# Optimization experiments

Measured on AMD Instinct MI355X. Metric: run time of the kernel, lower is better.

The kernel has to match this reference:

```python
import jax, jax.numpy as jnp
import numpy as np

NUM_LAYER = 5
EMB = 300
N_NODES = 100000
N_EDGES = 250000
BN_EPS = 1e-5


def setup_inputs() -> dict:
    key = jax.random.key(0)
    ks = jax.random.split(key, 12)
    s = 0.05
    inp = {
        "x": jax.random.randint(ks[0], (N_NODES, 2), 0, 3),
        "edge_index": jax.random.randint(ks[1], (2, N_EDGES), 0, N_NODES),
        "edge_attr": jax.random.randint(ks[2], (N_EDGES, 2), 0, 3),
        # node-feature embedding tables
        "x_emb1": jax.random.normal(ks[3], (120, EMB), jnp.float32) * s,
        "x_emb2": jax.random.normal(ks[4], (3, EMB), jnp.float32) * s,
        # per-layer edge embedding tables (bond type=6, bond direction=3)
        "e_emb1": jax.random.normal(ks[5], (NUM_LAYER, 6, EMB), jnp.float32) * s,
        "e_emb2": jax.random.normal(ks[6], (NUM_LAYER, 3, EMB), jnp.float32) * s,
        # per-layer GIN MLP: Linear(D,2D) -> ReLU -> Linear(2D,D); weights stored (out,in)
        "w1": jax.random.normal(ks[7], (NUM_LAYER, 2 * EMB, EMB), jnp.float32) * s,
        "b1": jnp.zeros((NUM_LAYER, 2 * EMB), jnp.float32),
        "w2": jax.random.normal(ks[8], (NUM_LAYER, EMB, 2 * EMB), jnp.float32) * s,
        "b2": jnp.zeros((NUM_LAYER, EMB), jnp.float32),
        # per-layer BatchNorm1d affine params (training-mode batch stats)
        "gamma": jnp.ones((NUM_LAYER, EMB), jnp.float32),
        "beta": jnp.zeros((NUM_LAYER, EMB), jnp.float32),
    }
    return inp


def reference(x, edge_index, edge_attr, x_emb1, x_emb2, e_emb1, e_emb2, w1, b1, w2, b2, gamma, beta):
    n = x.shape[0]
    # input node embedding: atom type + chirality tag
    h = x_emb1[x[:, 0]] + x_emb2[x[:, 1]]  # [N, D]

    # add self loops (self-loop edge_attr = [4, 0])
    loop = jnp.arange(n, dtype=edge_index.dtype)
    src = jnp.concatenate([edge_index[0], loop])  # [E+N]
    dst = jnp.concatenate([edge_index[1], loop])
    ea0 = jnp.concatenate([edge_attr[:, 0], jnp.full((n,), 4, edge_attr.dtype)])
    ea1 = jnp.concatenate([edge_attr[:, 1], jnp.zeros((n,), edge_attr.dtype)])

    for l in range(NUM_LAYER):
        e = e_emb1[l][ea0] + e_emb2[l][ea1]           # [E+N, D] edge embeddings
        msg = h[src] + e                               # gather + message
        agg = jax.ops.segment_sum(msg, dst, num_segments=n)  # scatter-add aggregate
        hid = jnp.maximum(agg @ w1[l].T + b1[l], 0.0)  # GIN MLP
        h2 = hid @ w2[l].T + b2[l]
        # BatchNorm1d (training-mode batch statistics, biased variance)
        mu = h2.mean(axis=0)
        var = jnp.mean((h2 - mu) ** 2, axis=0)
        h2 = (h2 - mu) * jax.lax.rsqrt(var + BN_EPS) * gamma[l] + beta[l]
        if l < NUM_LAYER - 1:
            h2 = jnp.maximum(h2, 0.0)  # ReLU (dropout ratio = 0)
        h = h2

    # JK == 'last'
    return h
```

## Files before the change

### kernel.cpp

```cpp
#include <hip/hip_runtime.h>
#include <hip/hip_bf16.h>

#define DD 300
#define C4 75
#define AGS 320
#define BN_EPS 1e-5f

typedef _Float16 f16x8 __attribute__((ext_vector_type(8)));
typedef float f32x4 __attribute__((ext_vector_type(4)));

union PackH4 { _Float16 h[4]; uint2 u; };

__device__ __forceinline__ void gld_lds16(const void* g, void* lds) {
    __builtin_amdgcn_global_load_lds(
        (const __attribute__((address_space(1))) void*)g,
        (__attribute__((address_space(3))) void*)lds, 16, 0, 0);
}

__global__ __launch_bounds__(256) void embed_kernel(
    const int* __restrict__ x, const float* __restrict__ emb1,
    const float* __restrict__ emb2, float* __restrict__ h, int hs, int total4)
{
    int i = blockIdx.x * 256 + threadIdx.x;
    if (i >= total4) return;
    int node = i / C4, chunk = i - node * C4;
    int a = x[2 * node], b = x[2 * node + 1];
    int c = chunk << 2;
    float4 v1 = *(const float4*)(emb1 + (size_t)a * DD + c);
    float4 v2 = *(const float4*)(emb2 + (size_t)b * DD + c);
    float4 r;
    r.x = v1.x + v2.x; r.y = v1.y + v2.y; r.z = v1.z + v2.z; r.w = v1.w + v2.w;
    *(float4*)(h + (size_t)node * hs + c) = r;
}

__global__ __launch_bounds__(256) void build_ec_kernel(
    const float* __restrict__ e1, const float* __restrict__ e2, float* __restrict__ ec)
{
    int gid = blockIdx.x * 256 + threadIdx.x;
    if (gid >= 5 * 18 * DD) return;
    int l = gid / (18 * DD);
    int rem = gid - l * 18 * DD;
    int combo = rem / DD;
    int c = rem - combo * DD;
    int a0 = combo / 3, a1 = combo - a0 * 3;
    ec[gid] = e1[(size_t)l * 6 * DD + a0 * DD + c] + e2[(size_t)l * 3 * DD + a1 * DD + c];
}

__global__ __launch_bounds__(256) void deg_kernel(
    const int* __restrict__ ei, int* __restrict__ deg, int E)
{
    int e = blockIdx.x * 256 + threadIdx.x;
    if (e >= E) return;
    atomicAdd(&deg[ei[E + e]], 1);
}

__global__ __launch_bounds__(256) void scan1_kernel(
    const int* __restrict__ deg, int* __restrict__ pre, int* __restrict__ blockSum, int n)
{
    __shared__ int sa[256], sb[256];
    int t = threadIdx.x;
    int base = blockIdx.x * 1024 + t * 4;
    int v0 = (base + 0 < n) ? deg[base + 0] : 0;
    int v1 = (base + 1 < n) ? deg[base + 1] : 0;
    int v2 = (base + 2 < n) ? deg[base + 2] : 0;
    int v3 = (base + 3 < n) ? deg[base + 3] : 0;
    int tot = v0 + v1 + v2 + v3;
    sa[t] = tot;
    __syncthreads();
    int* src = sa; int* dst = sb;
    for (int off = 1; off < 256; off <<= 1) {
        int v = src[t];
        if (t >= off) v += src[t - off];
        dst[t] = v;
        __syncthreads();
        int* tmp = src; src = dst; dst = tmp;
    }
    int incl = src[t];
    int excl = incl - tot;
    if (base + 0 < n) pre[base + 0] = excl;
    if (base + 1 < n) pre[base + 1] = excl + v0;
    if (base + 2 < n) pre[base + 2] = excl + v0 + v1;
    if (base + 3 < n) pre[base + 3] = excl + v0 + v1 + v2;
    if (t == 255) blockSum[blockIdx.x] = incl;
}

__global__ __launch_bounds__(256) void scan2_kernel(int* __restrict__ blockSum, int nb)
{
    __shared__ int sa[256], sb[256];
    int t = threadIdx.x;
    int v = (t < nb) ? blockSum[t] : 0;
    sa[t] = v;
    __syncthreads();
    int* src = sa; int* dst = sb;
    for (int off = 1; off < 256; off <<= 1) {
        int x = src[t];
        if (t >= off) x += src[t - off];
        dst[t] = x;
        __syncthreads();
        int* tmp = src; src = dst; dst = tmp;
    }
    if (t < nb) blockSum[t] = src[t] - v;
}

__global__ __launch_bounds__(256) void scan3_kernel(
    const int* __restrict__ pre, const int* __restrict__ blockSum,
    int* __restrict__ rowPtr, int* __restrict__ cursor, int n, int E)
{
    int idx = blockIdx.x * 256 + threadIdx.x;
    if (idx > n) return;
    int v = (idx < n) ? pre[idx] + blockSum[idx >> 10] : E;
    rowPtr[idx] = v;
    if (idx < n) cursor[idx] = v;
}

__global__ __launch_bounds__(256) void fill_kernel(
    const int* __restrict__ ei, const int* __restrict__ ea,
    int* __restrict__ cursor, int* __restrict__ edges, int E)
{
    int e = blockIdx.x * 256 + threadIdx.x;
    if (e >= E) return;
    int src = ei[e];
    int dst = ei[E + e];
    int combo = ea[2 * e] * 3 + ea[2 * e + 1];
    int slot = atomicAdd(&cursor[dst], 1);
    edges[slot] = src | (combo << 18);
}

__global__ __launch_bounds__(256) void gather_kernel(
    const float* __restrict__ h, int hs, const int* __restrict__ rowPtr,
    const int* __restrict__ edges, const float* __restrict__ ec,
    const float* __restrict__ scale, const float* __restrict__ shift, int use_affine,
    _Float16* __restrict__ agg, int n)
{
    int gid = blockIdx.x * 256 + threadIdx.x;
    int node = gid / C4, ch = gid - node * C4;
    if (node >= n) return;
    int c = ch << 2;
    float4 sc, sh;
    if (use_affine) {
        sc = *(const float4*)(scale + c);
        sh = *(const float4*)(shift + c);
    }
    float4 acc = *(const float4*)(h + (size_t)node * hs + c);
    if (use_affine) {
        acc.x = fmaxf(fmaf(sc.x, acc.x, sh.x), 0.f);
        acc.y = fmaxf(fmaf(sc.y, acc.y, sh.y), 0.f);
        acc.z = fmaxf(fmaf(sc.z, acc.z, sh.z), 0.f);
        acc.w = fmaxf(fmaf(sc.w, acc.w, sh.w), 0.f);
    }
    float4 es = *(const float4*)(ec + 12 * DD + c);
    acc.x += es.x; acc.y += es.y; acc.z += es.z; acc.w += es.w;

    int start = rowPtr[node], end = rowPtr[node + 1];
    for (int e = start; e < end; ++e) {
        int pk = edges[e];
        int src = pk & 0x3FFFF;
        int combo = pk >> 18;
        float4 hv = *(const float4*)(h + (size_t)src * hs + c);
        if (use_affine) {
            hv.x = fmaxf(fmaf(sc.x, hv.x, sh.x), 0.f);
            hv.y = fmaxf(fmaf(sc.y, hv.y, sh.y), 0.f);
            hv.z = fmaxf(fmaf(sc.z, hv.z, sh.z), 0.f);
            hv.w = fmaxf(fmaf(sc.w, hv.w, sh.w), 0.f);
        }
        float4 ev = *(const float4*)(ec + combo * DD + c);
        acc.x += hv.x + ev.x;
        acc.y += hv.y + ev.y;
        acc.z += hv.z + ev.z;
        acc.w += hv.w + ev.w;
    }
    PackH4 p;
    p.h[0] = (_Float16)acc.x;
    p.h[1] = (_Float16)acc.y;
    p.h[2] = (_Float16)acc.z;
    p.h[3] = (_Float16)acc.w;
    *(uint2*)(agg + (size_t)node * AGS + c) = p.u;
}

__global__ __launch_bounds__(256) void convert_w_kernel(
    const float* __restrict__ w, _Float16* __restrict__ wf,
    int rows, int cols, int rowsP, int colsP)
{
    int gid = blockIdx.x * 256 + threadIdx.x;
    int total = 5 * rowsP * colsP;
    if (gid >= total) return;
    int l = gid / (rowsP * colsP);
    int rem = gid - l * (rowsP * colsP);
    int r = rem / colsP;
    int k = rem - r * colsP;
    float v = (r < rows && k < cols) ? w[((size_t)l * rows + r) * cols + k] : 0.f;
    wf[gid] = (_Float16)v;
}

template <bool OUT_F16, bool DO_STATS>
__global__ __launch_bounds__(512, 4) void mfma_gemm_lds(
    const _Float16* __restrict__ A, const _Float16* __restrict__ W,
    const float* __restrict__ bias,
    _Float16* __restrict__ outH, float* __restrict__ outF,
    float* __restrict__ sum, float* __restrict__ sumsq,
    int M, int Kp, int outStride, int outN, int nCol)
{
    __shared__ __attribute__((aligned(16))) unsigned short sA[128 * 64];
    __shared__ __attribute__((aligned(16))) unsigned short sB[128 * 64];

    const int bid = blockIdx.x;
    const int group = bid / (8 * nCol);
    const int within = bid - group * 8 * nCol;
    const int rowT = group * 8 + (within & 7);
    const int colT = within >> 3;
    const int bm = rowT << 7;
    const int bn = colT << 7;

    const int tid = threadIdx.x;
    const int lane = tid & 63, wv = tid >> 6;
    const int wy = wv & 3, wx = wv >> 2;
    const int quad = lane >> 4, l16 = lane & 15;

    const int r8 = lane >> 3;
    const int chv = (lane & 7) ^ r8;

    f32x4 acc[2][4] = {};

    for (int k0 = 0; k0 < Kp; k0 += 64) {
        __syncthreads();
#pragma unroll
        for (int j = 0; j < 2; ++j) {
            int rloc = wv * 16 + j * 8 + r8;
            gld_lds16(A + (size_t)(bm + rloc) * Kp + k0 + chv * 8,
                      &sA[(wv * 16 + j * 8) * 64]);
        }
#pragma unroll
        for (int j = 0; j < 2; ++j) {
            int rloc = wv * 16 + j * 8 + r8;
            gld_lds16(W + (size_t)(bn + rloc) * Kp + k0 + chv * 8,
                      &sB[(wv * 16 + j * 8) * 64]);
        }
        __syncthreads();
#pragma unroll
        for (int kk = 0; kk < 2; ++kk) {
            f16x8 a[2], b[4];
#pragma unroll
            for (int i = 0; i < 2; ++i) {
                int rA = wy * 32 + i * 16 + l16;
                int slotA = (kk * 4 + quad) ^ (rA & 7);
                a[i] = *(const f16x8*)&sA[rA * 64 + slotA * 8];
            }
#pragma unroll
            for (int j = 0; j < 4; ++j) {
                int rB = wx * 64 + j * 16 + l16;
                int slotB = (kk * 4 + quad) ^ (rB & 7);
                b[j] = *(const f16x8*)&sB[rB * 64 + slotB * 8];
            }
#pragma unroll
            for (int i = 0; i < 2; ++i)
#pragma unroll
                for (int j = 0; j < 4; ++j)
                    acc[i][j] = __builtin_amdgcn_mfma_f32_16x16x32_f16(
                        a[i], b[j], acc[i][j], 0, 0, 0);
        }
    }

#pragma unroll
    for (int j = 0; j < 4; ++j) {
        int col = bn + wx * 64 + j * 16 + l16;
        float bv = (col < outN) ? bias[col] : 0.f;
        float cs = 0.f, cq = 0.f;
#pragma unroll
        for (int i = 0; i < 2; ++i) {
            int rowBase = bm + wy * 32 + i * 16 + (quad << 2);
#pragma unroll
            for (int r = 0; r < 4; ++r) {
                int row = rowBase + r;
                if (row >= M) continue;
                float v = acc[i][j][r] + bv;
                if constexpr (DO_STATS) { if (col < outN) { cs += v; cq += v * v; } }
                if constexpr (OUT_F16) {
                    float o = (col < outN) ? fmaxf(v, 0.f) : 0.f;
                    outH[(size_t)row * outStride + col] = (_Float16)o;
                } else {
                    if (col < outStride) outF[(size_t)row * outStride + col] = v;
                }
            }
        }
        if constexpr (DO_STATS) {
            cs += __shfl_down(cs, 32); cq += __shfl_down(cq, 32);
            cs += __shfl_down(cs, 16); cq += __shfl_down(cq, 16);
            if (quad == 0 && col < outN) {
                atomicAdd(&sum[col], cs);
                atomicAdd(&sumsq[col], cq);
            }
        }
    }
}

__global__ void finalize_kernel(
    const float* __restrict__ sum, const float* __restrict__ sumsq,
    const float* __restrict__ gamma, const float* __restrict__ beta,
    float* __restrict__ scale, float* __restrict__ shift, float inv_n)
{
    int c = threadIdx.x;
    if (c < DD) {
        float mu = sum[c] * inv_n;
        float var = sumsq[c] * inv_n - mu * mu;
        float inv = rsqrtf(var + BN_EPS);
        float sc = gamma[c] * inv;
        scale[c] = sc;
        shift[c] = fmaf(-mu, sc, beta[c]);
    }
}

__global__ __launch_bounds__(256) void apply_kernel(
    const float* __restrict__ h, int hs, const float* __restrict__ scale,
    const float* __restrict__ shift, float* __restrict__ out, int total4)
{
    int i = blockIdx.x * 256 + threadIdx.x;
    if (i >= total4) return;
    int node = i / C4;
    int c = (i - node * C4) << 2;
    float4 v = *(const float4*)(h + (size_t)node * hs + c);
    float4 r;
    r.x = fmaf(scale[c + 0], v.x, shift[c + 0]);
    r.y = fmaf(scale[c + 1], v.y, shift[c + 1]);
    r.z = fmaf(scale[c + 2], v.z, shift[c + 2]);
    r.w = fmaf(scale[c + 3], v.w, shift[c + 3]);
    ((float4*)out)[i] = r;
}

extern "C" void kernel_launch(void* const* d_in, const int* in_sizes, int n_in,
                              void* d_out, int out_size, void* d_ws, size_t ws_size,
                              hipStream_t stream)
{
    const int*   x      = (const int*)d_in[0];
    const int*   ei     = (const int*)d_in[1];
    const int*   ea     = (const int*)d_in[2];
    const float* x_emb1 = (const float*)d_in[3];
    const float* x_emb2 = (const float*)d_in[4];
    const float* e_emb1 = (const float*)d_in[5];
    const float* e_emb2 = (const float*)d_in[6];
    const float* w1     = (const float*)d_in[7];
    const float* b1     = (const float*)d_in[8];
    const float* w2     = (const float*)d_in[9];
    const float* b2     = (const float*)d_in[10];
    const float* gamma  = (const float*)d_in[11];
    const float* beta   = (const float*)d_in[12];

    const int n = in_sizes[0] / 2;
    const int E = in_sizes[1] / 2;
    const int nRowT = (n + 127) / 128;
    const int nRowTP = ((nRowT + 7) / 8) * 8;
    const int MpA = nRowTP * 128;
    const int Kp1 = AGS, Kp2 = 640;
    const int NP1 = 640, NP2 = 384;

    char* p = (char*)d_ws;
    auto alloc = [&](size_t bytes) -> void* {
        void* r = (void*)p;
        p += (bytes + 255) & ~(size_t)255;
        return r;
    };
    _Float16* agg  = (_Float16*)alloc((size_t)MpA * Kp1 * 2);
    _Float16* hid  = (_Float16*)alloc((size_t)MpA * Kp2 * 2);
    _Float16* w1f  = (_Float16*)alloc((size_t)5 * NP1 * Kp1 * 2);
    _Float16* w2f  = (_Float16*)alloc((size_t)5 * NP2 * Kp2 * 2);
    float* ec     = (float*)alloc((size_t)5 * 18 * DD * 4);
    int*   deg    = (int*)alloc((size_t)n * 4);
    int*   rowPtr = (int*)alloc((size_t)(n + 1) * 4);
    int*   cursor = (int*)alloc((size_t)n * 4);
    int*   blockSum = (int*)alloc(256 * 4);
    int*   edges  = (int*)alloc((size_t)E * 4);
    float* sum   = (float*)alloc(320 * 4);
    float* sumsq = (float*)alloc(320 * 4);
    float* scale = (float*)alloc(320 * 4);
    float* shift = (float*)alloc(320 * 4);

    const size_t used = (size_t)(p - (char*)d_ws);
    const size_t hBytes = (size_t)n * 320 * 4;
    float* h;
    int HS;
    if (ws_size >= used + hBytes) {
        h = (float*)alloc(hBytes);
        HS = 320;
    } else {
        h = (float*)d_out;
        HS = DD;
    }

    const int total4 = n * C4;
    const int nb = (n + 1023) / 1024;

    {
        convert_w_kernel<<<(5 * NP1 * Kp1 + 255) / 256, 256, 0, stream>>>(w1, w1f, 600, 300, NP1, Kp1);
        convert_w_kernel<<<(5 * NP2 * Kp2 + 255) / 256, 256, 0, stream>>>(w2, w2f, 300, 600, NP2, Kp2);
        build_ec_kernel<<<(5 * 18 * DD + 255) / 256, 256, 0, stream>>>(e_emb1, e_emb2, ec);
        hipMemsetAsync(deg, 0, (size_t)n * 4, stream);
        deg_kernel<<<(E + 255) / 256, 256, 0, stream>>>(ei, deg, E);
        scan1_kernel<<<nb, 256, 0, stream>>>(deg, cursor , blockSum, n);
        scan2_kernel<<<1, 256, 0, stream>>>(blockSum, nb);
        scan3_kernel<<<(n + 256) / 256, 256, 0, stream>>>(cursor, blockSum, rowPtr, deg , n, E);
        fill_kernel<<<(E + 255) / 256, 256, 0, stream>>>(ei, ea, deg, edges, E);
        hipMemsetAsync(agg, 0, (size_t)MpA * Kp1 * 2, stream);
        embed_kernel<<<(total4 + 255) / 256, 256, 0, stream>>>(x, x_emb1, x_emb2, h, HS, total4);
    }

    const int gatherTotal = n * C4;
    const int nCol1 = NP1 / 128;
    const int nCol2 = NP2 / 128;
    const int g1 = nRowTP * nCol1;
    const int g2 = nRowTP * nCol2;

    for (int l = 0; l < 5; l++) {
        hipMemsetAsync(sum, 0, 2 * 320 * sizeof(float), stream);
        gather_kernel<<<(gatherTotal + 255) / 256, 256, 0, stream>>>(
            h, HS, rowPtr, edges, ec + (size_t)l * 18 * DD, scale, shift, l > 0 ? 1 : 0,
            agg, n);
        mfma_gemm_lds<true, false><<<g1, 512, 0, stream>>>(
            agg, w1f + (size_t)l * NP1 * Kp1,
            b1 + (size_t)l * 600, hid, nullptr, nullptr, nullptr,
            n, Kp1, Kp2, 600, nCol1);
        mfma_gemm_lds<false, true><<<g2, 512, 0, stream>>>(
            hid, w2f + (size_t)l * NP2 * Kp2,
            b2 + (size_t)l * 300, nullptr, h, sum, sumsq,
            n, Kp2, HS, 300, nCol2);
        finalize_kernel<<<1, 320, 0, stream>>>(sum, sumsq, gamma + (size_t)l * DD,
                                               beta + (size_t)l * DD, scale, shift,
                                               1.0f / (float)n);
    }
    apply_kernel<<<(total4 + 255) / 256, 256, 0, stream>>>(h, HS, scale, shift,
                                                           (float*)d_out, total4);
}
```

Measured before the change: 1.875 ms.

## Double-buffer LDS tiles in MFMA GEMM to overlap global loads with compute

Splits the GEMM K-loop into stage and compute steps over two LDS buffers, so the next K tile is prefetched with direct global-to-LDS loads while the current tile feeds the MFMAs. Explicit vmcnt waits and raw barriers replace the two __syncthreads per iteration. LDS use per block doubles to 64KB and the occupancy hint drops from 4 to 2 blocks per CU, which may reduce latency hiding across blocks.

```diff
diff --git a/kernel.cpp b/kernel.cpp
--- a/kernel.cpp
+++ b/kernel.cpp
@@ -193,15 +193,15 @@
 }
 
 template <bool OUT_F16, bool DO_STATS>
-__global__ __launch_bounds__(512, 4) void mfma_gemm_lds(
+__global__ __launch_bounds__(512, 2) void mfma_gemm_lds(
     const _Float16* __restrict__ A, const _Float16* __restrict__ W,
     const float* __restrict__ bias,
     _Float16* __restrict__ outH, float* __restrict__ outF,
     float* __restrict__ sum, float* __restrict__ sumsq,
     int M, int Kp, int outStride, int outN, int nCol)
 {
-    __shared__ __attribute__((aligned(16))) unsigned short sA[128 * 64];
-    __shared__ __attribute__((aligned(16))) unsigned short sB[128 * 64];
+    __shared__ __attribute__((aligned(16))) unsigned short sA[2][128 * 64];
+    __shared__ __attribute__((aligned(16))) unsigned short sB[2][128 * 64];
 
     const int bid = blockIdx.x;
     const int group = bid / (8 * nCol);
@@ -221,21 +221,22 @@
 
     f32x4 acc[2][4] = {};
 
-    for (int k0 = 0; k0 < Kp; k0 += 64) {
-        __syncthreads();
+    auto STAGE = [&](int buf, int k0) {
 #pragma unroll
         for (int j = 0; j < 2; ++j) {
             int rloc = wv * 16 + j * 8 + r8;
             gld_lds16(A + (size_t)(bm + rloc) * Kp + k0 + chv * 8,
-                      &sA[(wv * 16 + j * 8) * 64]);
+                      &sA[buf][(wv * 16 + j * 8) * 64]);
         }
 #pragma unroll
         for (int j = 0; j < 2; ++j) {
             int rloc = wv * 16 + j * 8 + r8;
             gld_lds16(W + (size_t)(bn + rloc) * Kp + k0 + chv * 8,
-                      &sB[(wv * 16 + j * 8) * 64]);
-        }
-        __syncthreads();
+                      &sB[buf][(wv * 16 + j * 8) * 64]);
+        }
+    };
+
+    auto COMPUTE = [&](int buf) {
 #pragma unroll
         for (int kk = 0; kk < 2; ++kk) {
             f16x8 a[2], b[4];
@@ -243,13 +244,13 @@
             for (int i = 0; i < 2; ++i) {
                 int rA = wy * 32 + i * 16 + l16;
                 int slotA = (kk * 4 + quad) ^ (rA & 7);
-                a[i] = *(const f16x8*)&sA[rA * 64 + slotA * 8];
+                a[i] = *(const f16x8*)&sA[buf][rA * 64 + slotA * 8];
             }
 #pragma unroll
             for (int j = 0; j < 4; ++j) {
                 int rB = wx * 64 + j * 16 + l16;
                 int slotB = (kk * 4 + quad) ^ (rB & 7);
-                b[j] = *(const f16x8*)&sB[rB * 64 + slotB * 8];
+                b[j] = *(const f16x8*)&sB[buf][rB * 64 + slotB * 8];
             }
 #pragma unroll
             for (int i = 0; i < 2; ++i)
@@ -258,6 +259,22 @@
                     acc[i][j] = __builtin_amdgcn_mfma_f32_16x16x32_f16(
                         a[i], b[j], acc[i][j], 0, 0, 0);
         }
+    };
+
+    const int nT = Kp >> 6;
+    STAGE(0, 0);
+    for (int t = 0; t < nT; ++t) {
+        if (t + 1 < nT) {
+            STAGE((t + 1) & 1, (t + 1) << 6);
+            asm volatile("s_waitcnt vmcnt(4)" ::: "memory");
+        } else {
+            asm volatile("s_waitcnt vmcnt(0)" ::: "memory");
+        }
+        __builtin_amdgcn_s_barrier();
+        __builtin_amdgcn_sched_barrier(0);
+        COMPUTE(t & 1);
+        __builtin_amdgcn_s_barrier();
+        __builtin_amdgcn_sched_barrier(0);
     }
 
 #pragma unroll
```

After: 1.879 ms. About the same (+0.2%).
